# Kernel tuning notes

Measured on AMD Instinct MI355X. Metric: run time of the kernel, lower is better.

The kernel has to match this reference:

```python
import jax, jax.numpy as jnp
import numpy as np

N_LOW, N_HIGH = 20000, 60000
E_LOW, E_L2H, E_HIGH = 320000, 540000, 480000
EPS = 1e-5
NEG_SLOPE = 0.2


def _gatv2(x_src, x_dst, edge_index, Wl, Wr, att, bias):
    """PyG GATv2Conv with concat heads, aggr='mean', no self loops.
    att: [H, C]. Returns [n_dst, H*C]."""
    H, C = att.shape
    n_dst = x_dst.shape[0]
    xl = (x_src @ Wl).reshape(-1, H, C)   # [n_src, H, C]
    xr = (x_dst @ Wr).reshape(-1, H, C)   # [n_dst, H, C]
    src, dst = edge_index[0], edge_index[1]
    z = jax.nn.leaky_relu(xl[src] + xr[dst], NEG_SLOPE)        # [E, H, C]
    logits = jnp.einsum('ehc,hc->eh', z, att)                  # [E, H]
    m = jax.ops.segment_max(logits, dst, num_segments=n_dst)   # segment softmax
    e = jnp.exp(logits - m[dst])
    s = jax.ops.segment_sum(e, dst, num_segments=n_dst)
    alpha = e / s[dst]                                         # [E, H]
    out = jax.ops.segment_sum(xl[src] * alpha[:, :, None], dst, num_segments=n_dst)
    deg = jax.ops.segment_sum(jnp.ones((src.shape[0],), out.dtype), dst, num_segments=n_dst)
    out = out / jnp.maximum(deg, 1.0)[:, None, None]           # aggr='mean'
    out = out.reshape(n_dst, H * C)
    if bias is not None:
        out = out + bias
    return out


def _bn(x, g, b):
    mu = x.mean(axis=0)
    var = x.var(axis=0)
    return (x - mu) * jax.lax.rsqrt(var + EPS) * g + b


def _forward(x_low, x_high, z_std, e_low, e_l2h, e_high,
             l1_Wl, l1_Wr, l1_att, l1_b, bn1_g, bn1_b,
             l2_Wl, l2_Wr, l2_att, l2_b, bn2_g, bn2_b,
             l3_Wl, l3_Wr, l3_att, l3_b,
             lh_Wl, lh_Wr, lh_att,
             h1_Wl, h1_Wr, h1_att, h1_b, bn3_g, bn3_b,
             h2_Wl, h2_Wr, h2_att, h2_b, bn4_g, bn4_b,
             h3_Wl, h3_Wr, h3_att, h3_b):
    # low_net: GATv2(125->128,h2) -> BN(256) -> GATv2(256->128) -> BN(128) -> GATv2(128->128)
    h = _gatv2(x_low, x_low, e_low, l1_Wl, l1_Wr, l1_att, l1_b)
    h = _bn(h, bn1_g, bn1_b)
    h = _gatv2(h, h, e_low, l2_Wl, l2_Wr, l2_att, l2_b)
    h = _bn(h, bn2_g, bn2_b)
    h = _gatv2(h, h, e_low, l3_Wl, l3_Wr, l3_att, l3_b)
    # bipartite low2high: (encod_low[128], x_high[1]) -> 128, no bias
    eh = _gatv2(h, x_high, e_l2h, lh_Wl, lh_Wr, lh_att, None)
    eh = jnp.concatenate([z_std, eh], axis=-1)                 # [N_HIGH, 129]
    # high_net
    g = _gatv2(eh, eh, e_high, h1_Wl, h1_Wr, h1_att, h1_b)
    g = _bn(g, bn3_g, bn3_b)
    g = _gatv2(g, g, e_high, h2_Wl, h2_Wr, h2_att, h2_b)
    g = _bn(g, bn4_g, bn4_b)
    return _gatv2(g, g, e_high, h3_Wl, h3_Wr, h3_att, h3_b)   # [N_HIGH, 2]


def setup_inputs() -> dict:
    key = jax.random.key(0)
    ks = iter(jax.random.split(key, 64))
    def P(shape, fan_in):
        return jax.random.normal(next(ks), shape, jnp.float32) / np.sqrt(fan_in)
    inp = {}
    inp['x_low'] = jax.random.normal(next(ks), (N_LOW, 125), jnp.float32)
    inp['x_high'] = jax.random.normal(next(ks), (N_HIGH, 1), jnp.float32)
    inp['z_std'] = jax.random.normal(next(ks), (N_HIGH, 1), jnp.float32)
    inp['e_low'] = jnp.stack([jax.random.randint(next(ks), (E_LOW,), 0, N_LOW),
                              jax.random.randint(next(ks), (E_LOW,), 0, N_LOW)])
    inp['e_l2h'] = jnp.stack([jax.random.randint(next(ks), (E_L2H,), 0, N_LOW),
                              jax.random.randint(next(ks), (E_L2H,), 0, N_HIGH)])
    inp['e_high'] = jnp.stack([jax.random.randint(next(ks), (E_HIGH,), 0, N_HIGH),
                               jax.random.randint(next(ks), (E_HIGH,), 0, N_HIGH)])
    inp['l1_Wl'] = P((125, 256), 125); inp['l1_Wr'] = P((125, 256), 125)
    inp['l1_att'] = P((2, 128), 128);  inp['l1_b'] = jnp.zeros((256,), jnp.float32)
    inp['bn1_g'] = jnp.ones((256,), jnp.float32); inp['bn1_b'] = jnp.zeros((256,), jnp.float32)
    inp['l2_Wl'] = P((256, 128), 256); inp['l2_Wr'] = P((256, 128), 256)
    inp['l2_att'] = P((1, 128), 128);  inp['l2_b'] = jnp.zeros((128,), jnp.float32)
    inp['bn2_g'] = jnp.ones((128,), jnp.float32); inp['bn2_b'] = jnp.zeros((128,), jnp.float32)
    inp['l3_Wl'] = P((128, 128), 128); inp['l3_Wr'] = P((128, 128), 128)
    inp['l3_att'] = P((1, 128), 128);  inp['l3_b'] = jnp.zeros((128,), jnp.float32)
    inp['lh_Wl'] = P((128, 128), 128); inp['lh_Wr'] = P((1, 128), 1)
    inp['lh_att'] = P((1, 128), 128)
    inp['h1_Wl'] = P((129, 256), 129); inp['h1_Wr'] = P((129, 256), 129)
    inp['h1_att'] = P((2, 128), 128);  inp['h1_b'] = jnp.zeros((256,), jnp.float32)
    inp['bn3_g'] = jnp.ones((256,), jnp.float32); inp['bn3_b'] = jnp.zeros((256,), jnp.float32)
    inp['h2_Wl'] = P((256, 128), 256); inp['h2_Wr'] = P((256, 128), 256)
    inp['h2_att'] = P((1, 128), 128);  inp['h2_b'] = jnp.zeros((128,), jnp.float32)
    inp['bn4_g'] = jnp.ones((128,), jnp.float32); inp['bn4_b'] = jnp.zeros((128,), jnp.float32)
    inp['h3_Wl'] = P((128, 2), 128);   inp['h3_Wr'] = P((128, 2), 128)
    inp['h3_att'] = P((1, 2), 2);      inp['h3_b'] = jnp.zeros((2,), jnp.float32)
    return inp


def reference(x_low, x_high, z_std, e_low, e_l2h, e_high,
              l1_Wl, l1_Wr, l1_att, l1_b, bn1_g, bn1_b,
              l2_Wl, l2_Wr, l2_att, l2_b, bn2_g, bn2_b,
              l3_Wl, l3_Wr, l3_att, l3_b,
              lh_Wl, lh_Wr, lh_att,
              h1_Wl, h1_Wr, h1_att, h1_b, bn3_g, bn3_b,
              h2_Wl, h2_Wr, h2_att, h2_b, bn4_g, bn4_b,
              h3_Wl, h3_Wr, h3_att, h3_b):
    return _forward(x_low, x_high, z_std, e_low, e_l2h, e_high,
                    l1_Wl, l1_Wr, l1_att, l1_b, bn1_g, bn1_b,
                    l2_Wl, l2_Wr, l2_att, l2_b, bn2_g, bn2_b,
                    l3_Wl, l3_Wr, l3_att, l3_b,
                    lh_Wl, lh_Wr, lh_att,
                    h1_Wl, h1_Wr, h1_att, h1_b, bn3_g, bn3_b,
                    h2_Wl, h2_Wr, h2_att, h2_b, bn4_g, bn4_b,
                    h3_Wl, h3_Wr, h3_att, h3_b)
```

## Files before the change

kernel.cpp:

```cpp
#include <hip/hip_runtime.h>
#include <hip/hip_bf16.h>
#include <cstdint>
#include <cstddef>
#include <cmath>

#define NEG_SLOPE 0.2f

#define PB  1024
#define CSH 10
#define CBS 1024
#define NBCMAX 160

using frag = __attribute__((ext_vector_type(8))) short;
using facc = __attribute__((ext_vector_type(4))) float;

__device__ __forceinline__ float bf_hi(unsigned u) {
    union { unsigned i; float f; } t; t.i = u & 0xffff0000u; return t.f;
}
__device__ __forceinline__ float bf_lo(unsigned u) {
    union { unsigned i; float f; } t; t.i = u << 16; return t.f;
}
__device__ __forceinline__ void unpack8(uint4 u, float* v) {
    v[0] = bf_lo(u.x); v[1] = bf_hi(u.x);
    v[2] = bf_lo(u.y); v[3] = bf_hi(u.y);
    v[4] = bf_lo(u.z); v[5] = bf_hi(u.z);
    v[6] = bf_lo(u.w); v[7] = bf_hi(u.w);
}

typedef const __attribute__((address_space(1))) void* gas_cptr;
typedef __attribute__((address_space(3))) void* las_ptr;
__device__ __forceinline__ void gload_lds16(const __hip_bfloat16* g, __hip_bfloat16* l) {
    __builtin_amdgcn_global_load_lds((gas_cptr)(const void*)g, (las_ptr)(void*)l, 16, 0, 0);
}

__global__ __launch_bounds__(256)
void msplitA(const int* __restrict__ s0, const int* __restrict__ d0, int E0,
             const int* __restrict__ s1, const int* __restrict__ d1, int E1,
             const int* __restrict__ s2, const int* __restrict__ d2, int E2,
             int nc0, int nc1, int nc2, int cap0, int cap1, int cap2,
             int* __restrict__ stage, int* __restrict__ cnt2) {
    __shared__ int hist[NBCMAX];
    __shared__ int rbase[NBCMAX];
    __shared__ int curs[NBCMAX];
    __shared__ int ord[1024];
    __shared__ int obkt[1024];
    const int NBC = nc0 + nc1 + nc2;
    const long Etot = (long)E0 + E1 + E2;
    int tid = threadIdx.x;
    int lane = tid & 63;
    long chunk = (Etot + PB - 1) / PB;
    long c0 = (long)blockIdx.x * chunk;
    long c1 = c0 + chunk; if (c1 > Etot) c1 = Etot;
    const long sec1 = (long)PB * nc0 * cap0;
    const long sec2 = sec1 + (long)PB * nc1 * cap1;
    for (int t = tid; t < NBC; t += 256) curs[t] = 0;
    __syncthreads();
    for (long r0 = c0; r0 < c1; r0 += 1024) {
        int n = (int)((c1 - r0 < 1024) ? (c1 - r0) : 1024);
        for (int t = tid; t < NBC; t += 256) hist[t] = 0;
        __syncthreads();
        int mye[4], myb[4], myr[4];
#pragma unroll
        for (int k = 0; k < 4; ++k) {
            int li = k * 256 + tid;
            myb[k] = -1;
            if (li < n) {
                long i = r0 + li;
                int src, dst, gb;
                if (i < E0) { src = s0[i]; dst = d0[i]; gb = dst >> CSH; }
                else if (i < (long)E0 + E1) { long j = i - E0; src = s1[j]; dst = d1[j]; gb = nc0 + (dst >> CSH); }
                else { long j = i - E0 - E1; src = s2[j]; dst = d2[j]; gb = nc0 + nc1 + (dst >> CSH); }
                mye[k] = (src << CSH) | (dst & (CBS - 1));
                myb[k] = gb;
                myr[k] = atomicAdd(&hist[gb], 1);
            }
        }
        __syncthreads();
        if (tid < 64) {
            int carry = 0;
            for (int base = 0; base < NBC; base += 64) {
                int g = base + lane;
                int v = (g < NBC) ? hist[g] : 0;
                int sum = v;
#pragma unroll
                for (int o = 1; o < 64; o <<= 1) {
                    int t = __shfl_up(sum, o, 64);
                    if (lane >= o) sum += t;
                }
                if (g < NBC) rbase[g] = carry + sum - v;
                carry += __shfl(sum, 63, 64);
            }
        }
        __syncthreads();
#pragma unroll
        for (int k = 0; k < 4; ++k)
            if (myb[k] >= 0) {
                int pos = rbase[myb[k]] + myr[k];
                ord[pos] = mye[k];
                obkt[pos] = myb[k];
            }
        __syncthreads();
        for (int pos = tid; pos < n; pos += 256) {
            int b = obkt[pos];
            int rank = pos - rbase[b] + curs[b];
            long addr; int cap;
            if (b < nc0)            { cap = cap0; addr = (long)(blockIdx.x * nc0 + b) * cap0; }
            else if (b < nc0 + nc1) { cap = cap1; addr = sec1 + (long)(blockIdx.x * nc1 + (b - nc0)) * cap1; }
            else                    { cap = cap2; addr = sec2 + (long)(blockIdx.x * nc2 + (b - nc0 - nc1)) * cap2; }
            if (rank < cap) stage[addr + rank] = ord[pos];
        }
        __syncthreads();
        for (int t = tid; t < NBC; t += 256) curs[t] += hist[t];
        __syncthreads();
    }
    for (int t = tid; t < NBC; t += 256) {
        int cap = (t < nc0) ? cap0 : (t < nc0 + nc1) ? cap1 : cap2;
        int c = curs[t]; if (c > cap) c = cap;
        cnt2[(long)blockIdx.x * NBC + t] = c;
    }
}

__global__ void scanC1(const int* __restrict__ cnt2, int* __restrict__ tot, int NBC) {
    __shared__ int red[256];
    int gb = blockIdx.x;
    int tid = threadIdx.x;
    int s = 0;
    for (int p = tid; p < PB; p += 256) s += cnt2[(long)p * NBC + gb];
    red[tid] = s;
    __syncthreads();
    for (int o = 128; o; o >>= 1) {
        if (tid < o) red[tid] += red[tid + o];
        __syncthreads();
    }
    if (tid == 0) tot[gb] = red[0];
}

__global__ void scanC2(const int* __restrict__ tot, int* __restrict__ cstart,
                       int NBC, int nc0, int nc1) {
    if (threadIdx.x == 0) {
        int c = 0;
        for (int gb = 0; gb < NBC; ++gb) {
            if (gb == nc0 || gb == nc0 + nc1) c = 0;
            cstart[gb] = c;
            c += tot[gb];
        }
    }
}

__global__ __launch_bounds__(1024)
void fineB(const int* __restrict__ cnt2, const int* __restrict__ cstart,
           const int* __restrict__ stage,
           int nc0, int nc1, int nc2, int cap0, int cap1, int cap2,
           int* __restrict__ off0, int* __restrict__ col0, int n0,
           int* __restrict__ off1, int* __restrict__ col1, int n1,
           int* __restrict__ off2, int* __restrict__ col2, int n2) {
    __shared__ int fragb[PB + 1];
    __shared__ int cnt[1024];
    __shared__ int wsum[17];
    const int NBC = nc0 + nc1 + nc2;
    int gb = blockIdx.x;
    int tid = threadIdx.x;
    int lane = tid & 63;
    int wv = tid >> 6;
    int cb, ncg, n; long base2, stride; int* off; int* col;
    const long sec1 = (long)PB * nc0 * cap0;
    const long sec2 = sec1 + (long)PB * nc1 * cap1;
    if (gb < nc0) {
        cb = gb; ncg = nc0; n = n0; off = off0; col = col0;
        base2 = (long)cb * cap0; stride = (long)nc0 * cap0;
    } else if (gb < nc0 + nc1) {
        cb = gb - nc0; ncg = nc1; n = n1; off = off1; col = col1;
        base2 = sec1 + (long)cb * cap1; stride = (long)nc1 * cap1;
    } else {
        cb = gb - nc0 - nc1; ncg = nc2; n = n2; off = off2; col = col2;
        base2 = sec2 + (long)cb * cap2; stride = (long)nc2 * cap2;
    }
    int dlo = cb << CSH;
    int colbase = cstart[gb];
    int v = cnt2[(long)tid * NBC + gb];
    int sum = v;
#pragma unroll
    for (int o = 1; o < 64; o <<= 1) {
        int t = __shfl_up(sum, o, 64);
        if (lane >= o) sum += t;
    }
    if (lane == 63) wsum[wv] = sum;
    __syncthreads();
    if (tid == 0) {
        int c = 0;
        for (int w = 0; w < 16; ++w) { int t = wsum[w]; wsum[w] = c; c += t; }
        wsum[16] = c;
    }
    __syncthreads();
    fragb[tid] = wsum[wv] + sum - v;
    if (tid == 0) fragb[PB] = wsum[16];
    __syncthreads();
    int sz = fragb[PB];
    cnt[tid] = 0;
    __syncthreads();
    for (int p = tid; p < sz; p += 1024) {
        int lo = 0, hi = PB;
        while (hi - lo > 1) { int mid = (lo + hi) >> 1; if (fragb[mid] <= p) lo = mid; else hi = mid; }
        int e = stage[base2 + (long)lo * stride + (p - fragb[lo])];
        atomicAdd(&cnt[e & (CBS - 1)], 1);
    }
    __syncthreads();
    int cv = cnt[tid];
    int csum = cv;
#pragma unroll
    for (int o = 1; o < 64; o <<= 1) {
        int t = __shfl_up(csum, o, 64);
        if (lane >= o) csum += t;
    }
    if (lane == 63) wsum[wv] = csum;
    __syncthreads();
    if (tid == 0) {
        int c = 0;
        for (int w = 0; w < 16; ++w) { int t = wsum[w]; wsum[w] = c; c += t; }
    }
    __syncthreads();
    int excl = wsum[wv] + csum - cv;
    int d = dlo + tid;
    if (d < n) off[d] = colbase + excl;
    if (cb == ncg - 1 && tid == 0) off[n] = colbase + sz;
    __syncthreads();
    cnt[tid] = colbase + excl;
    __syncthreads();
    for (int p = tid; p < sz; p += 1024) {
        int lo = 0, hi = PB;
        while (hi - lo > 1) { int mid = (lo + hi) >> 1; if (fragb[mid] <= p) lo = mid; else hi = mid; }
        int e = stage[base2 + (long)lo * stride + (p - fragb[lo])];
        int pos = atomicAdd(&cnt[e & (CBS - 1)], 1);
        col[pos] = e >> CSH;
    }
}

__global__ __launch_bounds__(256)
void gemm_bf16_mfma(const __hip_bfloat16* __restrict__ A,
                    const __hip_bfloat16* __restrict__ Bt,
                    __hip_bfloat16* __restrict__ C,
                    const float* __restrict__ bias, int M, int N, int Kp) {
    __shared__ __hip_bfloat16 As[128 * 32];
    __shared__ __hip_bfloat16 Bs[128 * 32];
    int tid = threadIdx.x;
    int lane = tid & 63;
    int wave = tid >> 6;
    int wm = wave >> 1, wn = wave & 1;
    int quad = lane >> 4, l16 = lane & 15;
    int m0 = blockIdx.y * 128;
    int n0 = blockIdx.x * 128;

    facc acc[4][4] = {};

    for (int k0 = 0; k0 < Kp; k0 += 32) {
#pragma unroll
        for (int p = 0; p < 2; ++p) {
            int idx = p * 256 + tid;
            int row = idx >> 2;
            int koff = (idx & 3) * 8;
            int gr = m0 + row; if (gr >= M) gr = M - 1;
            int lbase = (p * 256 + wave * 64) * 8;
            gload_lds16(A + (size_t)gr * Kp + k0 + koff, As + lbase);
            gload_lds16(Bt + (size_t)(n0 + row) * Kp + k0 + koff, Bs + lbase);
        }
        __syncthreads();

        frag a[4], b[4];
#pragma unroll
        for (int i = 0; i < 4; ++i) {
            a[i] = *reinterpret_cast<const frag*>(As + (wm * 64 + i * 16 + l16) * 32 + quad * 8);
            b[i] = *reinterpret_cast<const frag*>(Bs + (wn * 64 + i * 16 + l16) * 32 + quad * 8);
        }
#pragma unroll
        for (int i = 0; i < 4; ++i)
#pragma unroll
            for (int j = 0; j < 4; ++j)
                acc[i][j] = __builtin_amdgcn_mfma_f32_16x16x32_bf16(a[i], b[j], acc[i][j], 0, 0, 0);
        __syncthreads();
    }

#pragma unroll
    for (int i = 0; i < 4; ++i)
#pragma unroll
        for (int j = 0; j < 4; ++j) {
            int col = n0 + wn * 64 + j * 16 + l16;
            float bv = (bias != nullptr) ? bias[col] : 0.f;
#pragma unroll
            for (int r = 0; r < 4; ++r) {
                int row = m0 + wm * 64 + i * 16 + quad * 4 + r;
                if (row < M) C[(size_t)row * N + col] = __float2bfloat16(acc[i][j][r] + bv);
            }
        }
}

__global__ void gemm_n22_bn(const __hip_bfloat16* __restrict__ A,
                            const float* __restrict__ Wl, const float* __restrict__ Wr,
                            const float* __restrict__ s, const float* __restrict__ t,
                            float* __restrict__ YL, float* __restrict__ YR, int M, int K) {
    int i = blockIdx.x * blockDim.x + threadIdx.x;
    if (i >= M) return;
    float l0 = 0.f, l1 = 0.f, r0 = 0.f, r1 = 0.f;
    const unsigned* a = (const unsigned*)(A + (size_t)i * K);
    for (int k2 = 0; k2 < K / 2; ++k2) {
        unsigned u = a[k2];
        int k = k2 * 2;
        float v0 = fmaf(bf_lo(u), s[k], t[k]);
        float v1 = fmaf(bf_hi(u), s[k + 1], t[k + 1]);
        l0 = fmaf(v0, Wl[k * 2 + 0], l0);
        l1 = fmaf(v0, Wl[k * 2 + 1], l1);
        l0 = fmaf(v1, Wl[k * 2 + 2], l0);
        l1 = fmaf(v1, Wl[k * 2 + 3], l1);
        r0 = fmaf(v0, Wr[k * 2 + 0], r0);
        r1 = fmaf(v0, Wr[k * 2 + 1], r1);
        r0 = fmaf(v1, Wr[k * 2 + 2], r0);
        r1 = fmaf(v1, Wr[k * 2 + 3], r1);
    }
    YL[(size_t)i * 2 + 0] = l0;
    YL[(size_t)i * 2 + 1] = l1;
    YR[(size_t)i * 2 + 0] = r0;
    YR[(size_t)i * 2 + 1] = r1;
}

__global__ void prep_all(const float* __restrict__ l1Wl, const float* __restrict__ l1Wr,
                         const float* __restrict__ lhWl,
                         const float* __restrict__ h1Wl, const float* __restrict__ h1Wr,
                         const float* __restrict__ x_low, const float* __restrict__ x_high,
                         const float* __restrict__ lhWr, const float* __restrict__ z_std,
                         __hip_bfloat16* __restrict__ w_l1, __hip_bfloat16* __restrict__ w_lh,
                         __hip_bfloat16* __restrict__ w_h1,
                         __hip_bfloat16* __restrict__ XLOWB, __hip_bfloat16* __restrict__ XRo,
                         __hip_bfloat16* __restrict__ EHB,
                         int o1, int o2, int o3, int o4, int o5, int o6, int o7, int o8) {
    int i = blockIdx.x * blockDim.x + threadIdx.x;
    if (i < o1) {
        int r = i >> 7, c = i & 127;
        XLOWB[i] = __float2bfloat16((c < 125) ? x_low[(size_t)r * 125 + c] : 0.f);
    } else if (i < o2) {
        int j = i - o1; int r = j >> 7, c = j & 127;
        XRo[j] = __float2bfloat16(x_high[r] * lhWr[c]);
    } else if (i < o3) {
        int j = i - o2; int r = j >> 5, c = (j & 31) + 128;
        EHB[(size_t)r * 160 + c] = __float2bfloat16((c == 128) ? z_std[r] : 0.f);
    } else if (i < o4) {
        int j = i - o3; int n = j >> 7, k = j & 127;
        w_l1[j] = __float2bfloat16((k < 125) ? l1Wl[(size_t)k * 256 + n] : 0.f);
    } else if (i < o5) {
        int j = i - o4; int n = j >> 7, k = j & 127;
        w_l1[256 * 128 + j] = __float2bfloat16((k < 125) ? l1Wr[(size_t)k * 256 + n] : 0.f);
    } else if (i < o6) {
        int j = i - o5; int n = j >> 7, k = j & 127;
        w_lh[j] = __float2bfloat16(lhWl[(size_t)k * 128 + n]);
    } else if (i < o7) {
        int j = i - o6; int n = j / 160, k = j - n * 160;
        float v = 0.f;
        if (k < 128) v = h1Wl[(size_t)(k + 1) * 256 + n];
        else if (k == 128) v = h1Wl[n];
        w_h1[j] = __float2bfloat16(v);
    } else if (i < o8) {
        int j = i - o7; int n = j / 160, k = j - n * 160;
        float v = 0.f;
        if (k < 128) v = h1Wr[(size_t)(k + 1) * 256 + n];
        else if (k == 128) v = h1Wr[n];
        w_h1[256 * 160 + j] = __float2bfloat16(v);
    }
}

__global__ void wconv_bnfold2(const float* __restrict__ Wl, const float* __restrict__ Wr,
                              const float* __restrict__ scale, const float* __restrict__ shift,
                              __hip_bfloat16* __restrict__ Wt, float* __restrict__ bout,
                              int K, int N, int Kp) {
    __shared__ float red[256];
    const float* W = blockIdx.y ? Wr : Wl;
    __hip_bfloat16* wt = Wt + (size_t)blockIdx.y * N * Kp;
    float* bo = bout + blockIdx.y * N;
    int n = blockIdx.x;
    int tid = threadIdx.x;
    float acc = 0.f;
    for (int k = tid; k < Kp; k += 256) {
        float v = 0.f;
        if (k < K) {
            float w = W[(size_t)k * N + n];
            v = w * scale[k];
            acc = fmaf(w, shift[k], acc);
        }
        wt[(size_t)n * Kp + k] = __float2bfloat16(v);
    }
    red[tid] = acc;
    __syncthreads();
    for (int o = 128; o; o >>= 1) {
        if (tid < o) red[tid] += red[tid + o];
        __syncthreads();
    }
    if (tid == 0) bo[n] = red[0];
}

__global__ void gat_c128_v4(const __hip_bfloat16* __restrict__ xl, int xls,
                            const __hip_bfloat16* __restrict__ xr, int xrs,
                            const int* __restrict__ row_off, const int* __restrict__ col,
                            const float* __restrict__ att, const float* __restrict__ bias,
                            __hip_bfloat16* __restrict__ outb, int obstride,
                            int n_dst, int H) {
    int wid = (blockIdx.x * blockDim.x + threadIdx.x) >> 6;
    int lane = threadIdx.x & 63;
    int total = n_dst * H;
    if (wid >= total) return;
    int dst = wid / H;
    int h = wid - dst * H;
    int g = lane >> 4;
    int q = lane & 15;
    int cb = h * 128 + q * 8;
    int beg = row_off[dst], end = row_off[dst + 1];

    float xrv[8], av[8];
    unpack8(*(const uint4*)(xr + (size_t)dst * xrs + cb), xrv);
    {
        float4 a0 = *(const float4*)(att + cb);
        float4 a1 = *(const float4*)(att + cb + 4);
        av[0] = a0.x; av[1] = a0.y; av[2] = a0.z; av[3] = a0.w;
        av[4] = a1.x; av[5] = a1.y; av[6] = a1.z; av[7] = a1.w;
    }

    float s = 0.f;
    float acc[8] = {0.f, 0.f, 0.f, 0.f, 0.f, 0.f, 0.f, 0.f};

    if (beg < end) {
        int e0g = beg + g;
        bool pv = e0g < end;
        int i0 = col[pv ? e0g : beg];
        uint4 u = *(const uint4*)(xl + (size_t)i0 * xls + cb);
        int e1g = beg + 4 + g;
        int i1 = (beg + 4 < end) ? col[(e1g < end) ? e1g : beg] : 0;

        for (int e0 = beg; e0 < end; e0 += 4) {
            bool have_next = (e0 + 4) < end;
            uint4 un;
            if (have_next)
                un = *(const uint4*)(xl + (size_t)i1 * xls + cb);
            int e2g = e0 + 8 + g;
            int i2 = (e0 + 8 < end) ? col[(e2g < end) ? e2g : beg] : 0;
            bool nv = (e0 + 4 + g) < end;

            float v[8];
            unpack8(u, v);
            float p = 0.f;
#pragma unroll
            for (int c = 0; c < 8; ++c) {
                float z = v[c] + xrv[c];
                z = fmaxf(z, NEG_SLOPE * z);
                p = fmaf(z, av[c], p);
            }
            p += __shfl_xor(p, 8, 64);
            p += __shfl_xor(p, 4, 64);
            p += __shfl_xor(p, 2, 64);
            p += __shfl_xor(p, 1, 64);
            if (!pv) p = -INFINITY;
            float w = __expf(fminf(p, 85.f));
            s += w;
#pragma unroll
            for (int c = 0; c < 8; ++c) acc[c] = fmaf(w, v[c], acc[c]);

            if (have_next) { u = un; pv = nv; }
            i1 = i2;
        }
    }

#pragma unroll
    for (int o = 16; o <= 32; o <<= 1) {
        s += __shfl_xor(s, o, 64);
#pragma unroll
        for (int c = 0; c < 8; ++c) acc[c] += __shfl_xor(acc[c], o, 64);
    }

    int deg = end - beg;
    float inv = (deg > 0) ? 1.f / (s * (float)deg) : 0.f;
    float o8[8];
#pragma unroll
    for (int c = 0; c < 8; ++c) o8[c] = acc[c] * inv;
    if (bias != nullptr) {
#pragma unroll
        for (int c = 0; c < 8; ++c) o8[c] += bias[cb + c];
    }
    if (g == 0) {
        union { uint4 u; __hip_bfloat16 hh[8]; } pk;
#pragma unroll
        for (int c = 0; c < 8; ++c) pk.hh[c] = __float2bfloat16(o8[c]);
        *(uint4*)(outb + (size_t)dst * obstride + cb) = pk.u;
    }
}

__global__ void gat_c2(const float* __restrict__ xl, const float* __restrict__ xr,
                       const int* __restrict__ row_off, const int* __restrict__ col,
                       const float* __restrict__ att, const float* __restrict__ bias,
                       float* __restrict__ out, int n_dst) {
    int dst = blockIdx.x * blockDim.x + threadIdx.x;
    if (dst >= n_dst) return;
    float x0 = xr[(size_t)dst * 2], x1 = xr[(size_t)dst * 2 + 1];
    float a0 = att[0], a1 = att[1];
    int beg = row_off[dst], end = row_off[dst + 1];
    float s = 0.f, acc0 = 0.f, acc1 = 0.f;
    for (int e = beg; e < end; ++e) {
        int src = col[e];
        float v0 = xl[(size_t)src * 2], v1 = xl[(size_t)src * 2 + 1];
        float z0 = v0 + x0; z0 = fmaxf(z0, NEG_SLOPE * z0);
        float z1 = v1 + x1; z1 = fmaxf(z1, NEG_SLOPE * z1);
        float p = fmaf(z0, a0, z1 * a1);
        float w = __expf(fminf(p, 85.f));
        s += w;
        acc0 = fmaf(w, v0, acc0);
        acc1 = fmaf(w, v1, acc1);
    }
    int deg = end - beg;
    float o0 = 0.f, o1 = 0.f;
    if (deg > 0) {
        float inv = 1.f / (s * (float)deg);
        o0 = acc0 * inv;
        o1 = acc1 * inv;
    }
    out[(size_t)dst * 2 + 0] = o0 + bias[0];
    out[(size_t)dst * 2 + 1] = o1 + bias[1];
}

__global__ void bn_partial_d(const __hip_bfloat16* __restrict__ x, float* __restrict__ part,
                             int Nr, int rpb) {
    int C = blockDim.x;
    int c = threadIdx.x;
    int b = blockIdx.x;
    int r0 = b * rpb;
    int r1 = r0 + rpb; if (r1 > Nr) r1 = Nr;
    float s = 0.f, q = 0.f;
    for (int r = r0; r < r1; ++r) {
        float v = __bfloat162float(x[(size_t)r * C + c]);
        s += v;
        q = fmaf(v, v, q);
    }
    part[(size_t)b * C + c] = s;
    part[65536 + (size_t)b * C + c] = q;
}

__global__ void bn_finalize_w(const float* __restrict__ part,
                              const float* __restrict__ g, const float* __restrict__ b,
                              float* __restrict__ scale, float* __restrict__ shift,
                              int Nr, int C) {
    int c = (blockIdx.x * blockDim.x + threadIdx.x) >> 6;
    int lane = threadIdx.x & 63;
    if (c >= C) return;
    float s = 0.f, q = 0.f;
    for (int blk = lane; blk < 256; blk += 64) {
        s += part[(size_t)blk * C + c];
        q += part[65536 + (size_t)blk * C + c];
    }
#pragma unroll
    for (int o = 32; o; o >>= 1) {
        s += __shfl_xor(s, o, 64);
        q += __shfl_xor(q, o, 64);
    }
    if (lane == 0) {
        float mu = s / (float)Nr;
        float var = q / (float)Nr - mu * mu;
        float inv = rsqrtf(var + 1e-5f);
        float a = g[c] * inv;
        scale[c] = a;
        shift[c] = b[c] - mu * a;
    }
}

extern "C" void kernel_launch(void* const* d_in, const int* in_sizes, int n_in,
                              void* d_out, int out_size, void* d_ws, size_t ws_size,
                              hipStream_t stream) {
    const float* x_low  = (const float*)d_in[0];
    const float* x_high = (const float*)d_in[1];
    const float* z_std  = (const float*)d_in[2];
    const int* e_low  = (const int*)d_in[3];
    const int* e_l2h  = (const int*)d_in[4];
    const int* e_high = (const int*)d_in[5];
    const float* l1_Wl = (const float*)d_in[6];
    const float* l1_Wr = (const float*)d_in[7];
    const float* l1_att = (const float*)d_in[8];
    const float* l1_b  = (const float*)d_in[9];
    const float* bn1_g = (const float*)d_in[10];
    const float* bn1_b = (const float*)d_in[11];
    const float* l2_Wl = (const float*)d_in[12];
    const float* l2_Wr = (const float*)d_in[13];
    const float* l2_att = (const float*)d_in[14];
    const float* l2_b  = (const float*)d_in[15];
    const float* bn2_g = (const float*)d_in[16];
    const float* bn2_b = (const float*)d_in[17];
    const float* l3_Wl = (const float*)d_in[18];
    const float* l3_Wr = (const float*)d_in[19];
    const float* l3_att = (const float*)d_in[20];
    const float* l3_b  = (const float*)d_in[21];
    const float* lh_Wl = (const float*)d_in[22];
    const float* lh_Wr = (const float*)d_in[23];
    const float* lh_att = (const float*)d_in[24];
    const float* h1_Wl = (const float*)d_in[25];
    const float* h1_Wr = (const float*)d_in[26];
    const float* h1_att = (const float*)d_in[27];
    const float* h1_b  = (const float*)d_in[28];
    const float* bn3_g = (const float*)d_in[29];
    const float* bn3_b = (const float*)d_in[30];
    const float* h2_Wl = (const float*)d_in[31];
    const float* h2_Wr = (const float*)d_in[32];
    const float* h2_att = (const float*)d_in[33];
    const float* h2_b  = (const float*)d_in[34];
    const float* bn4_g = (const float*)d_in[35];
    const float* bn4_b = (const float*)d_in[36];
    const float* h3_Wl = (const float*)d_in[37];
    const float* h3_Wr = (const float*)d_in[38];
    const float* h3_att = (const float*)d_in[39];
    const float* h3_b  = (const float*)d_in[40];

    const int N_low = in_sizes[0] / 125;
    const int N_high = in_sizes[1];
    const int E_low = in_sizes[3] / 2;
    const int E_l2h = in_sizes[4] / 2;
    const int E_high = in_sizes[5] / 2;

    char* ws = (char*)d_ws;
    size_t woff = 0;
    auto walloc = [&](size_t bytes) -> void* {
        void* p = (void*)(ws + woff);
        woff += (bytes + 255) & ~(size_t)255;
        return p;
    };
    __hip_bfloat16* XLR = (__hip_bfloat16*)walloc((size_t)N_high * 512 * 2);
    __hip_bfloat16* A1  = (__hip_bfloat16*)walloc((size_t)N_high * 256 * 2);
    __hip_bfloat16* A2  = (__hip_bfloat16*)walloc((size_t)N_high * 128 * 2);
    __hip_bfloat16* XRo = (__hip_bfloat16*)walloc((size_t)N_high * 128 * 2);
    __hip_bfloat16* XLOWB = (__hip_bfloat16*)walloc((size_t)N_low * 128 * 2);
    __hip_bfloat16* EHB = (__hip_bfloat16*)walloc((size_t)N_high * 160 * 2);
    float* YL = (float*)walloc((size_t)N_high * 2 * 4);
    float* YR = (float*)walloc((size_t)N_high * 2 * 4);
    int* off_low  = (int*)walloc((size_t)(N_low + 1) * 4);
    int* col_low  = (int*)walloc((size_t)E_low * 4);
    int* off_l2h  = (int*)walloc((size_t)(N_high + 1) * 4);
    int* col_l2h  = (int*)walloc((size_t)E_l2h * 4);
    int* off_high = (int*)walloc((size_t)(N_high + 1) * 4);
    int* col_high = (int*)walloc((size_t)E_high * 4);
    const int nc0 = (N_low + CBS - 1) >> CSH;
    const int nc1 = (N_high + CBS - 1) >> CSH;
    const int nc2 = (N_high + CBS - 1) >> CSH;
    const int NBC = nc0 + nc1 + nc2;
    const long Etot = (long)E_low + E_l2h + E_high;
    const long chunk = (Etot + PB - 1) / PB;
    auto capf = [&](int ng) {
        double m = (double)chunk * CBS / ng;
        int c = (int)(m + 8.0 * sqrt(m) + 16.0);
        return (c + 15) & ~15;
    };
    const int cap0 = capf(N_low);
    const int cap1 = capf(N_high);
    const int cap2 = capf(N_high);
    int* cnt2   = (int*)walloc((size_t)PB * NBC * 4);
    int* cstart = (int*)walloc((size_t)(NBC + 1) * 4);
    int* ctot   = (int*)walloc((size_t)(NBC + 1) * 4);
    float* bnpart = (float*)walloc(2 * 256 * 256 * 4);
    float* bnsc   = (float*)walloc(512 * 4);
    float* bb     = (float*)walloc(512 * 4);
    __hip_bfloat16* w_l1 = (__hip_bfloat16*)walloc(512 * 128 * 2);
    __hip_bfloat16* w_l2 = (__hip_bfloat16*)walloc(256 * 256 * 2);
    __hip_bfloat16* w_l3 = (__hip_bfloat16*)walloc(256 * 128 * 2);
    __hip_bfloat16* w_lh = (__hip_bfloat16*)walloc(128 * 128 * 2);
    __hip_bfloat16* w_h1 = (__hip_bfloat16*)walloc(512 * 160 * 2);
    __hip_bfloat16* w_h2 = (__hip_bfloat16*)walloc(256 * 256 * 2);

    int* stage = (int*)XLR;

    {
        int o1 = N_low * 128;
        int o2 = o1 + N_high * 128;
        int o3 = o2 + N_high * 32;
        int o4 = o3 + 256 * 128;
        int o5 = o4 + 256 * 128;
        int o6 = o5 + 128 * 128;
        int o7 = o6 + 256 * 160;
        int o8 = o7 + 256 * 160;
        prep_all<<<(o8 + 255) / 256, 256, 0, stream>>>(
            l1_Wl, l1_Wr, lh_Wl, h1_Wl, h1_Wr, x_low, x_high, lh_Wr, z_std,
            w_l1, w_lh, w_h1, XLOWB, XRo, EHB,
            o1, o2, o3, o4, o5, o6, o7, o8);
    }

    msplitA<<<PB, 256, 0, stream>>>(
        e_low, e_low + E_low, E_low,
        e_l2h, e_l2h + E_l2h, E_l2h,
        e_high, e_high + E_high, E_high,
        nc0, nc1, nc2, cap0, cap1, cap2, stage, cnt2);
    scanC1<<<NBC, 256, 0, stream>>>(cnt2, ctot, NBC);
    scanC2<<<1, 64, 0, stream>>>(ctot, cstart, NBC, nc0, nc1);
    fineB<<<NBC, 1024, 0, stream>>>(cnt2, cstart, stage,
                                    nc0, nc1, nc2, cap0, cap1, cap2,
                                    off_low, col_low, N_low,
                                    off_l2h, col_l2h, N_high,
                                    off_high, col_high, N_high);

    auto gemm = [&](const __hip_bfloat16* A, const __hip_bfloat16* Bt, __hip_bfloat16* C,
                    int M, int N, int Kp, const float* bias) {
        dim3 g(N / 128, (M + 127) / 128);
        gemm_bf16_mfma<<<g, 256, 0, stream>>>(A, Bt, C, bias, M, N, Kp);
    };
    auto gat = [&](const __hip_bfloat16* xl, int xls, const __hip_bfloat16* xr, int xrs,
                   const int* roff, const int* colv,
                   const float* att, const float* bias,
                   __hip_bfloat16* outb, int obs, int n_dst, int H) {
        long thr = (long)n_dst * H * 64;
        gat_c128_v4<<<(unsigned)((thr + 255) / 256), 256, 0, stream>>>(
            xl, xls, xr, xrs, roff, colv, att, bias, outb, obs, n_dst, H);
    };
    auto bn_stats = [&](__hip_bfloat16* x, const float* g, const float* b, int Nr, int C) {
        int rpb = (Nr + 255) / 256;
        bn_partial_d<<<256, C, 0, stream>>>(x, bnpart, Nr, rpb);
        bn_finalize_w<<<(C * 64 + 255) / 256, 256, 0, stream>>>(bnpart, g, b, bnsc, bnsc + 256, Nr, C);
    };
    auto fold2 = [&](const float* Wl, const float* Wr, __hip_bfloat16* Wt,
                     int K, int Nn, int Kp) {
        dim3 g(Nn, 2);
        wconv_bnfold2<<<g, 256, 0, stream>>>(Wl, Wr, bnsc, bnsc + 256, Wt, bb, K, Nn, Kp);
    };

    gemm(XLOWB, w_l1, XLR, N_low, 512, 128, nullptr);
    gat(XLR, 512, XLR + 256, 512, off_low, col_low, l1_att, l1_b, A1, 256, N_low, 2);
    bn_stats(A1, bn1_g, bn1_b, N_low, 256);

    fold2(l2_Wl, l2_Wr, w_l2, 256, 128, 256);
    gemm(A1, w_l2, XLR, N_low, 256, 256, bb);
    gat(XLR, 256, XLR + 128, 256, off_low, col_low, l2_att, l2_b, A2, 128, N_low, 1);
    bn_stats(A2, bn2_g, bn2_b, N_low, 128);

    fold2(l3_Wl, l3_Wr, w_l3, 128, 128, 128);
    gemm(A2, w_l3, XLR, N_low, 256, 128, bb);
    gat(XLR, 256, XLR + 128, 256, off_low, col_low, l3_att, l3_b, A1, 128, N_low, 1);

    gemm(A1, w_lh, XLR, N_low, 128, 128, nullptr);
    gat(XLR, 128, XRo, 128, off_l2h, col_l2h, lh_att, nullptr, EHB, 160, N_high, 1);

    gemm(EHB, w_h1, XLR, N_high, 512, 160, nullptr);
    gat(XLR, 512, XLR + 256, 512, off_high, col_high, h1_att, h1_b, A1, 256, N_high, 2);
    bn_stats(A1, bn3_g, bn3_b, N_high, 256);

    fold2(h2_Wl, h2_Wr, w_h2, 256, 128, 256);
    gemm(A1, w_h2, XLR, N_high, 256, 256, bb);
    gat(XLR, 256, XLR + 128, 256, off_high, col_high, h2_att, h2_b, A2, 128, N_high, 1);
    bn_stats(A2, bn4_g, bn4_b, N_high, 128);

    gemm_n22_bn<<<(N_high + 255) / 256, 256, 0, stream>>>(A2, h3_Wl, h3_Wr,
                                                          bnsc, bnsc + 256, YL, YR, N_high, 128);
    gat_c2<<<(N_high + 255) / 256, 256, 0, stream>>>(YL, YR, off_high, col_high,
                                                     h3_att, h3_b, (float*)d_out, N_high);
}
```

Before: 750.8 us.

## Fuse BN finalize into weight fold and add dedicated two-head GAT kernel

Removes the separate bn_finalize launch before each weight fold: every fold block now reduces the 256 partial BN sums itself, computes scale and shift into shared memory, then folds them into the weights. Adds a specialized two-head GAT kernel where one wavefront covers both heads of a destination (32 lanes × 8 channels), instead of launching one wavefront per head. The fold kernel now redundantly repeats the partial reduction in every block (256 serial loads per thread), which trades launch overhead for extra global reads.

```diff
diff --git a/kernel.cpp b/kernel.cpp
--- a/kernel.cpp
+++ b/kernel.cpp
@@ -366,22 +366,39 @@
 }
 
 __global__ void wconv_bnfold2(const float* __restrict__ Wl, const float* __restrict__ Wr,
-                              const float* __restrict__ scale, const float* __restrict__ shift,
+                              const float* __restrict__ part,
+                              const float* __restrict__ g, const float* __restrict__ b,
+                              int Nr,
                               __hip_bfloat16* __restrict__ Wt, float* __restrict__ bout,
                               int K, int N, int Kp) {
     __shared__ float red[256];
+    __shared__ float sc[256], sh[256];
     const float* W = blockIdx.y ? Wr : Wl;
     __hip_bfloat16* wt = Wt + (size_t)blockIdx.y * N * Kp;
     float* bo = bout + blockIdx.y * N;
     int n = blockIdx.x;
     int tid = threadIdx.x;
+    if (tid < K) {
+        float s = 0.f, q = 0.f;
+        for (int blk = 0; blk < 256; ++blk) {
+            s += part[(size_t)blk * K + tid];
+            q += part[65536 + (size_t)blk * K + tid];
+        }
+        float mu = s / (float)Nr;
+        float var = q / (float)Nr - mu * mu;
+        float inv = rsqrtf(var + 1e-5f);
+        float a = g[tid] * inv;
+        sc[tid] = a;
+        sh[tid] = b[tid] - mu * a;
+    }
+    __syncthreads();
     float acc = 0.f;
     for (int k = tid; k < Kp; k += 256) {
         float v = 0.f;
         if (k < K) {
             float w = W[(size_t)k * N + n];
-            v = w * scale[k];
-            acc = fmaf(w, shift[k], acc);
+            v = w * sc[k];
+            acc = fmaf(w, sh[k], acc);
         }
         wt[(size_t)n * Kp + k] = __float2bfloat16(v);
     }
@@ -470,6 +487,94 @@
 #pragma unroll
         for (int c = 0; c < 8; ++c) acc[c] += __shfl_xor(acc[c], o, 64);
     }
+
+    int deg = end - beg;
+    float inv = (deg > 0) ? 1.f / (s * (float)deg) : 0.f;
+    float o8[8];
+#pragma unroll
+    for (int c = 0; c < 8; ++c) o8[c] = acc[c] * inv;
+    if (bias != nullptr) {
+#pragma unroll
+        for (int c = 0; c < 8; ++c) o8[c] += bias[cb + c];
+    }
+    if (g == 0) {
+        union { uint4 u; __hip_bfloat16 hh[8]; } pk;
+#pragma unroll
+        for (int c = 0; c < 8; ++c) pk.hh[c] = __float2bfloat16(o8[c]);
+        *(uint4*)(outb + (size_t)dst * obstride + cb) = pk.u;
+    }
+}
+
+__global__ void gat_c256h2(const __hip_bfloat16* __restrict__ xl, int xls,
+                           const __hip_bfloat16* __restrict__ xr, int xrs,
+                           const int* __restrict__ row_off, const int* __restrict__ col,
+                           const float* __restrict__ att, const float* __restrict__ bias,
+                           __hip_bfloat16* __restrict__ outb, int obstride,
+                           int n_dst) {
+    int dst = (blockIdx.x * blockDim.x + threadIdx.x) >> 6;
+    int lane = threadIdx.x & 63;
+    if (dst >= n_dst) return;
+    int g = lane >> 5;
+    int q = lane & 31;
+    int cb = q * 8;
+    int beg = row_off[dst], end = row_off[dst + 1];
+
+    float xrv[8], av[8];
+    unpack8(*(const uint4*)(xr + (size_t)dst * xrs + cb), xrv);
+    {
+        float4 a0 = *(const float4*)(att + cb);
+        float4 a1 = *(const float4*)(att + cb + 4);
+        av[0] = a0.x; av[1] = a0.y; av[2] = a0.z; av[3] = a0.w;
+        av[4] = a1.x; av[5] = a1.y; av[6] = a1.z; av[7] = a1.w;
+    }
+
+    float s = 0.f;
+    float acc[8] = {0.f, 0.f, 0.f, 0.f, 0.f, 0.f, 0.f, 0.f};
+
+    if (beg < end) {
+        int e0g = beg + g;
+        bool pv = e0g < end;
+        int i0 = col[pv ? e0g : beg];
+        uint4 u = *(const uint4*)(xl + (size_t)i0 * xls + cb);
+        int e1g = beg + 2 + g;
+        int i1 = (beg + 2 < end) ? col[(e1g < end) ? e1g : beg] : 0;
+
+        for (int e0 = beg; e0 < end; e0 += 2) {
+            bool have_next = (e0 + 2) < end;
+            uint4 un;
+            if (have_next)
+                un = *(const uint4*)(xl + (size_t)i1 * xls + cb);
+            int e2g = e0 + 4 + g;
+            int i2 = (e0 + 4 < end) ? col[(e2g < end) ? e2g : beg] : 0;
+            bool nv = (e0 + 2 + g) < end;
+
+            float v[8];
+            unpack8(u, v);
+            float p = 0.f;
+#pragma unroll
+            for (int c = 0; c < 8; ++c) {
+                float z = v[c] + xrv[c];
+                z = fmaxf(z, NEG_SLOPE * z);
+                p = fmaf(z, av[c], p);
+            }
+            p += __shfl_xor(p, 8, 64);
+            p += __shfl_xor(p, 4, 64);
+            p += __shfl_xor(p, 2, 64);
+            p += __shfl_xor(p, 1, 64);
+            if (!pv) p = -INFINITY;
+            float w = __expf(fminf(p, 85.f));
+            s += w;
+#pragma unroll
+            for (int c = 0; c < 8; ++c) acc[c] = fmaf(w, v[c], acc[c]);
+
+            if (have_next) { u = un; pv = nv; }
+            i1 = i2;
+        }
+    }
+
+    s += __shfl_xor(s, 32, 64);
+#pragma unroll
+    for (int c = 0; c < 8; ++c) acc[c] += __shfl_xor(acc[c], 32, 64);
 
     int deg = end - beg;
     float inv = (deg > 0) ? 1.f / (s * (float)deg) : 0.f;
@@ -698,50 +803,59 @@
         dim3 g(N / 128, (M + 127) / 128);
         gemm_bf16_mfma<<<g, 256, 0, stream>>>(A, Bt, C, bias, M, N, Kp);
     };
-    auto gat = [&](const __hip_bfloat16* xl, int xls, const __hip_bfloat16* xr, int xrs,
-                   const int* roff, const int* colv,
-                   const float* att, const float* bias,
-                   __hip_bfloat16* outb, int obs, int n_dst, int H) {
-        long thr = (long)n_dst * H * 64;
+    auto gat1 = [&](const __hip_bfloat16* xl, int xls, const __hip_bfloat16* xr, int xrs,
+                    const int* roff, const int* colv,
+                    const float* att, const float* bias,
+                    __hip_bfloat16* outb, int obs, int n_dst) {
+        long thr = (long)n_dst * 64;
         gat_c128_v4<<<(unsigned)((thr + 255) / 256), 256, 0, stream>>>(
-            xl, xls, xr, xrs, roff, colv, att, bias, outb, obs, n_dst, H);
+            xl, xls, xr, xrs, roff, colv, att, bias, outb, obs, n_dst, 1);
     };
-    auto bn_stats = [&](__hip_bfloat16* x, const float* g, const float* b, int Nr, int C) {
+    auto gat2 = [&](const __hip_bfloat16* xl, int xls, const __hip_bfloat16* xr, int xrs,
+                    const int* roff, const int* colv,
+                    const float* att, const float* bias,
+                    __hip_bfloat16* outb, int obs, int n_dst) {
+        long thr = (long)n_dst * 64;
+        gat_c256h2<<<(unsigned)((thr + 255) / 256), 256, 0, stream>>>(
+            xl, xls, xr, xrs, roff, colv, att, bias, outb, obs, n_dst);
+    };
+    auto bn_partial = [&](__hip_bfloat16* x, int Nr, int C) {
         int rpb = (Nr + 255) / 256;
         bn_partial_d<<<256, C, 0, stream>>>(x, bnpart, Nr, rpb);
-        bn_finalize_w<<<(C * 64 + 255) / 256, 256, 0, stream>>>(bnpart, g, b, bnsc, bnsc + 256, Nr, C);
     };
-    auto fold2 = [&](const float* Wl, const float* Wr, __hip_bfloat16* Wt,
-                     int K, int Nn, int Kp) {
-        dim3 g(Nn, 2);
-        wconv_bnfold2<<<g, 256, 0, stream>>>(Wl, Wr, bnsc, bnsc + 256, Wt, bb, K, Nn, Kp);
+    auto fold2 = [&](const float* Wl, const float* Wr, const float* g, const float* b,
+                     int Nr, __hip_bfloat16* Wt, int K, int Nn, int Kp) {
+        dim3 gr(Nn, 2);
+        wconv_bnfold2<<<gr, 256, 0, stream>>>(Wl, Wr, bnpart, g, b, Nr, Wt, bb, K, Nn, Kp);
     };
 
     gemm(XLOWB, w_l1, XLR, N_low, 512, 128, nullptr);
-    gat(XLR, 512, XLR + 256, 512, off_low, col_low, l1_att, l1_b, A1, 256, N_low, 2);
-    bn_stats(A1, bn1_g, bn1_b, N_low, 256);
-
-    fold2(l2_Wl, l2_Wr, w_l2, 256, 128, 256);
+    gat2(XLR, 512, XLR + 256, 512, off_low, col_low, l1_att, l1_b, A1, 256, N_low);
+    bn_partial(A1, N_low, 256);
+
+    fold2(l2_Wl, l2_Wr, bn1_g, bn1_b, N_low, w_l2, 256, 128, 256);
     gemm(A1, w_l2, XLR, N_low, 256, 256, bb);
-    gat(XLR, 256, XLR + 128, 256, off_low, col_low, l2_att, l2_b, A2, 128, N_low, 1);
-    bn_stats(A2, bn2_g, bn2_b, N_low, 128);
-
-    fold2(l3_Wl, l3_Wr, w_l3, 128, 128, 128);
+    gat1(XLR, 256, XLR + 128, 256, off_low, col_low, l2_att, l2_b, A2, 128, N_low);
+    bn_partial(A2, N_low, 128);
+
+    fold2(l3_Wl, l3_Wr, bn2_g, bn2_b, N_low, w_l3, 128, 128, 128);
     gemm(A2, w_l3, XLR, N_low, 256, 128, bb);
-    gat(XLR, 256, XLR + 128, 256, off_low, col_low, l3_att, l3_b, A1, 128, N_low, 1);
+    gat1(XLR, 256, XLR + 128, 256, off_low, col_low, l3_att, l3_b, A1, 128, N_low);
 
     gemm(A1, w_lh, XLR, N_low, 128, 128, nullptr);
-    gat(XLR, 128, XRo, 128, off_l2h, col_l2h, lh_att, nullptr, EHB, 160, N_high, 1);
+    gat1(XLR, 128, XRo, 128, off_l2h, col_l2h, lh_att, nullptr, EHB, 160, N_high);
 
     gemm(EHB, w_h1, XLR, N_high, 512, 160, nullptr);
-    gat(XLR, 512, XLR + 256, 512, off_high, col_high, h1_att, h1_b, A1, 256, N_high, 2);
-    bn_stats(A1, bn3_g, bn3_b, N_high, 256);
-
-    fold2(h2_Wl, h2_Wr, w_h2, 256, 128, 256);
+    gat2(XLR, 512, XLR + 256, 512, off_high, col_high, h1_att, h1_b, A1, 256, N_high);
+    bn_partial(A1, N_high, 256);
+
+    fold2(h2_Wl, h2_Wr, bn3_g, bn3_b, N_high, w_h2, 256, 128, 256);
     gemm(A1, w_h2, XLR, N_high, 256, 256, bb);
-    gat(XLR, 256, XLR + 128, 256, off_high, col_high, h2_att, h2_b, A2, 128, N_high, 1);
-    bn_stats(A2, bn4_g, bn4_b, N_high, 128);
-
+    gat1(XLR, 256, XLR + 128, 256, off_high, col_high, h2_att, h2_b, A2, 128, N_high);
+    bn_partial(A2, N_high, 128);
+
+    bn_finalize_w<<<(128 * 64 + 255) / 256, 256, 0, stream>>>(bnpart, bn4_g, bn4_b,
+                                                              bnsc, bnsc + 256, N_high, 128);
     gemm_n22_bn<<<(N_high + 255) / 256, 256, 0, stream>>>(A2, h3_Wl, h3_Wr,
                                                           bnsc, bnsc + 256, YL, YR, N_high, 128);
     gat_c2<<<(N_high + 255) / 256, 256, 0, stream>>>(YL, YR, off_high, col_high,
```

Result: slower. 787.5 us (+4.9%).
